# Optimization experiments

Hardware: AMD Instinct MI355X
Metric: run time of the kernel (lower is better)

Reference implementation:

```python
import jax, jax.numpy as jnp
import numpy as np

B, M, P, W = 128, 10000, 64, 24


def setup_inputs() -> dict:
    key = jax.random.key(0)
    k1, k2, k3 = jax.random.split(key, 3)
    x = jax.random.normal(k1, (B, M, P), dtype=jnp.float32)
    weight = jax.random.normal(k2, (M, P, W), dtype=jnp.float32)
    bound = 1.0 / np.sqrt(P)
    bias = jax.random.uniform(k3, (M, W), dtype=jnp.float32, minval=-bound, maxval=bound)
    return {"x": x, "weight": weight, "bias": bias}


def reference(x, weight, bias):
    # Per-channel linear: out[b, w, j] = sum_p x[b, j, p] * weight[j, p, w] + bias[j, w]
    # Replaces the original python loop of m tiny GEMMs with one batched contraction.
    out = jnp.einsum('bjp,jpw->bwj', x, weight) + bias.T[None, :, :]  # [B, W, M]
    return out
```

## Files before the change

### kernel.cpp

```cpp
#include <hip/hip_runtime.h>


constexpr int B  = 128;
constexpr int M  = 10000;
constexpr int P  = 64;
constexpr int W  = 24;

constexpr int JT  = 16;
constexpr int BH  = 16;
constexpr int NT  = 512;
constexpr int NWG = (M / JT) * (B / BH);

using bf8   = __attribute__((ext_vector_type(8))) __bf16;
using f32x4 = __attribute__((ext_vector_type(4))) float;

__device__ __forceinline__ unsigned short rne_bf16(float f) {
  const unsigned u = __float_as_uint(f);
  return (unsigned short)((u + 0x7fffu + ((u >> 16) & 1u)) >> 16);
}

__global__ __launch_bounds__(NT, 4) void pcl_kernel(
    const float* __restrict__ x, const float* __restrict__ wgt,
    const float* __restrict__ bias, float* __restrict__ out) {
  __shared__ __align__(16) char smem[81920];
  unsigned short* wsh  = reinterpret_cast<unsigned short*>(smem);
  unsigned short* xsh  = reinterpret_cast<unsigned short*>(smem + 49152);
  float*          obuf = reinterpret_cast<float*>(smem);

  const int t = threadIdx.x;

  const int orig = blockIdx.x;
  const int wgid = (orig & 7) * (NWG / 8) + (orig >> 3);
  const int jt = wgid >> 3;
  const int by = wgid & 7;
  const int j0 = jt * JT;
  const int b0 = by * BH;

  {
    const float4* wg4 = reinterpret_cast<const float4*>(wgt);
#pragma unroll
    for (int i = 0; i < 12; ++i) {
      const int s  = t + i * NT;
      const int j  = s / 384;
      const int rr = s - j * 384;
      const int p  = rr / 6;
      const int w4 = (rr - 6 * p) * 4;
      const float4 v = wg4[(size_t)(j0 + j) * 384 + rr];
      const float vv[4] = {v.x, v.y, v.z, v.w};
#pragma unroll
      for (int k = 0; k < 4; ++k) {
        const int w = w4 + k;
        wsh[((j * W + w) << 6) + (((p >> 3) ^ (w & 7)) << 3) + (p & 7)] =
            rne_bf16(vv[k]);
      }
    }
  }

  {
#pragma unroll
    for (int i = 0; i < 8; ++i) {
      const int g   = t + i * NT;
      const int b   = g >> 8;
      const int rem = g & 255;
      const int j   = rem >> 4;
      const int c2  = rem & 15;
      const float4 v = *reinterpret_cast<const float4*>(
          x + ((size_t)(b0 + b) * M + j0 + j) * P + 4 * c2);
      const unsigned u0 = (unsigned)rne_bf16(v.x) | ((unsigned)rne_bf16(v.y) << 16);
      const unsigned u1 = (unsigned)rne_bf16(v.z) | ((unsigned)rne_bf16(v.w) << 16);
      const int s = (c2 >> 1) ^ (b & 7);
      uint2* dst = reinterpret_cast<uint2*>(
          xsh + (((b << 4) + j) << 6) + (s << 3) + ((c2 & 1) << 2));
      *dst = uint2{u0, u1};
    }
  }

  const int wk   = t >> 6;
  const int lane = t & 63;
  const int col  = lane & 15;
  const int kg   = lane >> 4;

  f32x4 acc[2][2];
#pragma unroll
  for (int jj = 0; jj < 2; ++jj) {
    const int j = j0 + wk + 8 * jj;
#pragma unroll
    for (int nt = 0; nt < 2; ++nt) {
      const int w = nt * 16 + col;
      const float bv = (w < W) ? bias[(size_t)j * W + w] : 0.0f;
      acc[jj][nt] = f32x4{bv, bv, bv, bv};
    }
  }

  __syncthreads();

#pragma unroll
  for (int jj = 0; jj < 2; ++jj) {
    const int jl = wk + 8 * jj;
#pragma unroll
    for (int ks = 0; ks < 2; ++ks) {
      const int c = ks * 4 + kg;
      const bf8 af = *reinterpret_cast<const bf8*>(
          xsh + (((col << 4) + jl) << 6) + ((c ^ (col & 7)) << 3));
      bf8 bfr[2];
#pragma unroll
      for (int nt = 0; nt < 2; ++nt) {
        const int w  = nt * 16 + col;
        const int wr = (w < W) ? w : 0;
        bf8 v = *reinterpret_cast<const bf8*>(
            wsh + ((jl * W + wr) << 6) + ((c ^ (wr & 7)) << 3));
        if (w >= W) {
#pragma unroll
          for (int e = 0; e < 8; ++e) v[e] = (__bf16)0.0f;
        }
        bfr[nt] = v;
      }
#pragma unroll
      for (int nt = 0; nt < 2; ++nt)
        acc[jj][nt] = __builtin_amdgcn_mfma_f32_16x16x32_bf16(
            af, bfr[nt], acc[jj][nt], 0, 0, 0);
    }
  }

  __syncthreads();
#pragma unroll
  for (int jj = 0; jj < 2; ++jj) {
    const int jl = wk + 8 * jj;
#pragma unroll
    for (int nt = 0; nt < 2; ++nt) {
      const int w = nt * 16 + col;
      if (w < W) {
#pragma unroll
        for (int reg = 0; reg < 4; ++reg) {
          const int brow = kg * 4 + reg;
          obuf[(jl * 16 + brow) * 25 + w] = acc[jj][nt][reg];
        }
      }
    }
  }
  __syncthreads();
#pragma unroll
  for (int it = 0; it < 3; ++it) {
    const int d    = t + it * NT;
    const int jq   = d & 3;
    const int rest = d >> 2;
    const int w    = rest % 24;
    const int br   = rest / 24;
    float4 o;
    o.x = obuf[((4 * jq + 0) * 16 + br) * 25 + w];
    o.y = obuf[((4 * jq + 1) * 16 + br) * 25 + w];
    o.z = obuf[((4 * jq + 2) * 16 + br) * 25 + w];
    o.w = obuf[((4 * jq + 3) * 16 + br) * 25 + w];
    *reinterpret_cast<float4*>(
        out + ((size_t)(b0 + br) * W + w) * M + j0 + 4 * jq) = o;
  }
}

extern "C" void kernel_launch(void* const* d_in, const int* in_sizes, int n_in,
                              void* d_out, int out_size, void* d_ws, size_t ws_size,
                              hipStream_t stream) {
  const float* x    = (const float*)d_in[0];
  const float* wgt  = (const float*)d_in[1];
  const float* bias = (const float*)d_in[2];
  float* out        = (float*)d_out;

  dim3 grid(NWG);
  dim3 block(NT);
  hipLaunchKernelGGL(pcl_kernel, grid, block, 0, stream, x, wgt, bias, out);
}
```

Baseline: 125.6 us.

## Loop each workgroup over four batch chunks with register-prefetched x and reused weights

```diff
diff --git a/kernel.cpp b/kernel.cpp
--- a/kernel.cpp
+++ b/kernel.cpp
@@ -8,8 +8,9 @@
 
 constexpr int JT  = 16;
 constexpr int BH  = 16;
+constexpr int NCH = 4;
 constexpr int NT  = 512;
-constexpr int NWG = (M / JT) * (B / BH);
+constexpr int NWG = (M / JT) * (B / (BH * NCH));
 
 using bf8   = __attribute__((ext_vector_type(8))) __bf16;
 using f32x4 = __attribute__((ext_vector_type(4))) float;
@@ -25,16 +26,44 @@
   __shared__ __align__(16) char smem[81920];
   unsigned short* wsh  = reinterpret_cast<unsigned short*>(smem);
   unsigned short* xsh  = reinterpret_cast<unsigned short*>(smem + 49152);
-  float*          obuf = reinterpret_cast<float*>(smem);
+  float*          obuf = reinterpret_cast<float*>(smem + 49152);
 
   const int t = threadIdx.x;
 
   const int orig = blockIdx.x;
-  const int wgid = (orig & 7) * (NWG / 8) + (orig >> 3);
-  const int jt = wgid >> 3;
-  const int by = wgid & 7;
-  const int j0 = jt * JT;
-  const int b0 = by * BH;
+  const int xcd  = orig & 7;
+  const int idx  = orig >> 3;
+  const int wgid = (xcd < 2 ? xcd * 157 : 314 + (xcd - 2) * 156) + idx;
+  const int jt    = wgid >> 1;
+  const int bbase = (wgid & 1) * (BH * NCH);
+  const int j0    = jt * JT;
+
+  const int wk   = t >> 6;
+  const int lane = t & 63;
+  const int col  = lane & 15;
+  const int kg   = lane >> 4;
+
+  float bv[2][2];
+#pragma unroll
+  for (int jj = 0; jj < 2; ++jj) {
+    const int j = j0 + wk + 8 * jj;
+#pragma unroll
+    for (int nt = 0; nt < 2; ++nt) {
+      const int w = nt * 16 + col;
+      bv[jj][nt] = (w < W) ? bias[(size_t)j * W + w] : 0.0f;
+    }
+  }
+
+  float4 nx[8];
+#pragma unroll
+  for (int i = 0; i < 8; ++i) {
+    const int g   = t + i * NT;
+    const int b   = g >> 8;
+    const int j   = (g >> 4) & 15;
+    const int c2  = g & 15;
+    nx[i] = *reinterpret_cast<const float4*>(
+        x + ((size_t)(bbase + b) * M + j0 + j) * P + 4 * c2);
+  }
 
   {
     const float4* wg4 = reinterpret_cast<const float4*>(wgt);
@@ -56,103 +85,107 @@
     }
   }
 
-  {
+  for (int c = 0; c < NCH; ++c) {
+    if (c > 0) __syncthreads();
+
 #pragma unroll
     for (int i = 0; i < 8; ++i) {
-      const int g   = t + i * NT;
-      const int b   = g >> 8;
-      const int rem = g & 255;
-      const int j   = rem >> 4;
-      const int c2  = rem & 15;
-      const float4 v = *reinterpret_cast<const float4*>(
-          x + ((size_t)(b0 + b) * M + j0 + j) * P + 4 * c2);
-      const unsigned u0 = (unsigned)rne_bf16(v.x) | ((unsigned)rne_bf16(v.y) << 16);
-      const unsigned u1 = (unsigned)rne_bf16(v.z) | ((unsigned)rne_bf16(v.w) << 16);
+      const int g  = t + i * NT;
+      const int b  = g >> 8;
+      const int j  = (g >> 4) & 15;
+      const int c2 = g & 15;
+      const unsigned u0 =
+          (unsigned)rne_bf16(nx[i].x) | ((unsigned)rne_bf16(nx[i].y) << 16);
+      const unsigned u1 =
+          (unsigned)rne_bf16(nx[i].z) | ((unsigned)rne_bf16(nx[i].w) << 16);
       const int s = (c2 >> 1) ^ (b & 7);
-      uint2* dst = reinterpret_cast<uint2*>(
-          xsh + (((b << 4) + j) << 6) + (s << 3) + ((c2 & 1) << 2));
-      *dst = uint2{u0, u1};
-    }
-  }
-
-  const int wk   = t >> 6;
-  const int lane = t & 63;
-  const int col  = lane & 15;
-  const int kg   = lane >> 4;
-
-  f32x4 acc[2][2];
-#pragma unroll
-  for (int jj = 0; jj < 2; ++jj) {
-    const int j = j0 + wk + 8 * jj;
-#pragma unroll
-    for (int nt = 0; nt < 2; ++nt) {
-      const int w = nt * 16 + col;
-      const float bv = (w < W) ? bias[(size_t)j * W + w] : 0.0f;
-      acc[jj][nt] = f32x4{bv, bv, bv, bv};
-    }
-  }
-
-  __syncthreads();
-
-#pragma unroll
-  for (int jj = 0; jj < 2; ++jj) {
-    const int jl = wk + 8 * jj;
-#pragma unroll
-    for (int ks = 0; ks < 2; ++ks) {
-      const int c = ks * 4 + kg;
-      const bf8 af = *reinterpret_cast<const bf8*>(
-          xsh + (((col << 4) + jl) << 6) + ((c ^ (col & 7)) << 3));
-      bf8 bfr[2];
+      *reinterpret_cast<uint2*>(xsh + (((b << 4) + j) << 6) + (s << 3) +
+                                ((c2 & 1) << 2)) = uint2{u0, u1};
+    }
+
+    if (c < NCH - 1) {
+      const int b0n = bbase + (c + 1) * BH;
+#pragma unroll
+      for (int i = 0; i < 8; ++i) {
+        const int g   = t + i * NT;
+        const int b   = g >> 8;
+        const int j   = (g >> 4) & 15;
+        const int c2  = g & 15;
+        nx[i] = *reinterpret_cast<const float4*>(
+            x + ((size_t)(b0n + b) * M + j0 + j) * P + 4 * c2);
+      }
+    }
+
+    __syncthreads();
+
+    f32x4 acc[2][2];
+#pragma unroll
+    for (int jj = 0; jj < 2; ++jj)
+#pragma unroll
+      for (int nt = 0; nt < 2; ++nt)
+        acc[jj][nt] = f32x4{bv[jj][nt], bv[jj][nt], bv[jj][nt], bv[jj][nt]};
+
+#pragma unroll
+    for (int jj = 0; jj < 2; ++jj) {
+      const int jl = wk + 8 * jj;
+#pragma unroll
+      for (int ks = 0; ks < 2; ++ks) {
+        const int cc = ks * 4 + kg;
+        const bf8 af = *reinterpret_cast<const bf8*>(
+            xsh + (((col << 4) + jl) << 6) + ((cc ^ (col & 7)) << 3));
+        bf8 bfr[2];
+#pragma unroll
+        for (int nt = 0; nt < 2; ++nt) {
+          const int w  = nt * 16 + col;
+          const int wr = (w < W) ? w : 0;
+          bf8 v = *reinterpret_cast<const bf8*>(
+              wsh + ((jl * W + wr) << 6) + ((cc ^ (wr & 7)) << 3));
+          if (w >= W) {
+#pragma unroll
+            for (int e = 0; e < 8; ++e) v[e] = (__bf16)0.0f;
+          }
+          bfr[nt] = v;
+        }
+#pragma unroll
+        for (int nt = 0; nt < 2; ++nt)
+          acc[jj][nt] = __builtin_amdgcn_mfma_f32_16x16x32_bf16(
+              af, bfr[nt], acc[jj][nt], 0, 0, 0);
+      }
+    }
+
+    __syncthreads();
+
+#pragma unroll
+    for (int jj = 0; jj < 2; ++jj) {
+      const int jl = wk + 8 * jj;
 #pragma unroll
       for (int nt = 0; nt < 2; ++nt) {
-        const int w  = nt * 16 + col;
-        const int wr = (w < W) ? w : 0;
-        bf8 v = *reinterpret_cast<const bf8*>(
-            wsh + ((jl * W + wr) << 6) + ((c ^ (wr & 7)) << 3));
-        if (w >= W) {
-#pragma unroll
-          for (int e = 0; e < 8; ++e) v[e] = (__bf16)0.0f;
+        const int w = nt * 16 + col;
+        if (w < W) {
+#pragma unroll
+          for (int reg = 0; reg < 4; ++reg)
+            obuf[(jl * 16 + kg * 4 + reg) * 25 + w] = acc[jj][nt][reg];
         }
-        bfr[nt] = v;
-      }
-#pragma unroll
-      for (int nt = 0; nt < 2; ++nt)
-        acc[jj][nt] = __builtin_amdgcn_mfma_f32_16x16x32_bf16(
-            af, bfr[nt], acc[jj][nt], 0, 0, 0);
-    }
-  }
-
-  __syncthreads();
-#pragma unroll
-  for (int jj = 0; jj < 2; ++jj) {
-    const int jl = wk + 8 * jj;
-#pragma unroll
-    for (int nt = 0; nt < 2; ++nt) {
-      const int w = nt * 16 + col;
-      if (w < W) {
-#pragma unroll
-        for (int reg = 0; reg < 4; ++reg) {
-          const int brow = kg * 4 + reg;
-          obuf[(jl * 16 + brow) * 25 + w] = acc[jj][nt][reg];
-        }
-      }
-    }
-  }
-  __syncthreads();
-#pragma unroll
-  for (int it = 0; it < 3; ++it) {
-    const int d    = t + it * NT;
-    const int jq   = d & 3;
-    const int rest = d >> 2;
-    const int w    = rest % 24;
-    const int br   = rest / 24;
-    float4 o;
-    o.x = obuf[((4 * jq + 0) * 16 + br) * 25 + w];
-    o.y = obuf[((4 * jq + 1) * 16 + br) * 25 + w];
-    o.z = obuf[((4 * jq + 2) * 16 + br) * 25 + w];
-    o.w = obuf[((4 * jq + 3) * 16 + br) * 25 + w];
-    *reinterpret_cast<float4*>(
-        out + ((size_t)(b0 + br) * W + w) * M + j0 + 4 * jq) = o;
+      }
+    }
+    __syncthreads();
+
+    const int b0c = bbase + c * BH;
+#pragma unroll
+    for (int it = 0; it < 3; ++it) {
+      const int d    = t + it * NT;
+      const int jq   = d & 3;
+      const int rest = d >> 2;
+      const int w    = rest % 24;
+      const int br   = rest / 24;
+      float4 o;
+      o.x = obuf[((4 * jq + 0) * 16 + br) * 25 + w];
+      o.y = obuf[((4 * jq + 1) * 16 + br) * 25 + w];
+      o.z = obuf[((4 * jq + 2) * 16 + br) * 25 + w];
+      o.w = obuf[((4 * jq + 3) * 16 + br) * 25 + w];
+      *reinterpret_cast<float4*>(
+          out + ((size_t)(b0c + br) * W + w) * M + j0 + 4 * jq) = o;
+    }
   }
 }
 
```

After: 119.6 us. -4.7%, faster.
